# Kernel tuning notes

Measured on AMD Instinct MI355X. Metric: run time of the kernel, lower is better.

The kernel has to match this reference:

```python
import jax, jax.numpy as jnp
import numpy as np

N_SRC = 100000
N_DST = 20000
E = 640000
IN_FEATS = 256
NUM_HEADS = 4
OUT_FEATS = 32
NEG_SLOPE = 0.2


def setup_inputs() -> dict:
    key = jax.random.key(0)
    ks = jax.random.split(key, 8)
    x = jax.random.normal(ks[0], (N_SRC, IN_FEATS), dtype=jnp.float32)
    src_idx = jax.random.randint(ks[1], (E,), 0, N_SRC)
    dst_idx = jax.random.randint(ks[2], (E,), 0, N_DST)
    dst_to_src = jax.random.randint(ks[3], (N_DST,), 0, N_SRC)
    # parameters (xavier-ish scale)
    W = jax.random.normal(ks[4], (IN_FEATS, NUM_HEADS * OUT_FEATS), dtype=jnp.float32) * (1.0 / np.sqrt(IN_FEATS))
    attn_l = jax.random.normal(ks[5], (NUM_HEADS, OUT_FEATS), dtype=jnp.float32) * 0.1
    attn_r = jax.random.normal(ks[6], (NUM_HEADS, OUT_FEATS), dtype=jnp.float32) * 0.1
    return {"x": x, "W": W, "attn_l": attn_l, "attn_r": attn_r,
            "src_idx": src_idx, "dst_idx": dst_idx, "dst_to_src": dst_to_src}


def reference(x, W, attn_l, attn_r, src_idx, dst_idx, dst_to_src):
    # fc + reshape to heads: [N_src, H, D]
    h = (x @ W).reshape(N_SRC, NUM_HEADS, OUT_FEATS)
    # per-src-node left attention score: [N_src, H]
    el = jnp.einsum('nhd,hd->nh', h, attn_l)
    # self_gather: dst nodes are a subset of src nodes
    h_dst = h[dst_to_src]                       # [N_dst, H, D]
    er = jnp.einsum('nhd,hd->nh', h_dst, attn_r)  # [N_dst, H]
    # apply_edge + leaky_relu: per-edge scores [E, H]
    e = el[src_idx] + er[dst_idx]
    e = jnp.where(e >= 0, e, NEG_SLOPE * e)
    # NOTE: original code normalizes leaky_relu(e) directly (no exp)
    sum_e = jax.ops.segment_sum(e, dst_idx, num_segments=N_DST)  # [N_dst, H]
    attention = e / sum_e[dst_idx]              # [E, H]
    # attention_gather: weighted scatter-add of src features to dst
    msg = attention[:, :, None] * h[src_idx]    # [E, H, D]
    out = jax.ops.segment_sum(msg, dst_idx, num_segments=N_DST)  # [N_dst, H, D]
    return out
```

## Files before the change

### kernel.cpp

```cpp
#include <hip/hip_runtime.h>

#define N_SRC 100000
#define N_DST 20000
#define NE 640000
#define IN_F 256
#define NH 4
#define DF 32
#define NCOL 128

__global__ void k_prep(const float* __restrict__ W,
                       const float* __restrict__ attn_l,
                       const float* __restrict__ attn_r,
                       double* __restrict__ Wlr_t,
                       int* __restrict__ cnt) {
    int k = threadIdx.x;
    for (int j = 0; j < 8; ++j) {
        const float* attn = (j < 4) ? attn_l : attn_r;
        int hh = j & 3;
        double s = 0.0;
        for (int d = 0; d < DF; ++d)
            s += (double)W[k * NCOL + hh * DF + d] * (double)attn[hh * DF + d];
        Wlr_t[(size_t)j * IN_F + k] = s;
    }
    for (int i = k; i < N_DST; i += 256) cnt[i] = 0;
}

__global__ __launch_bounds__(512) void k_gemm(const float* __restrict__ x,
                                              const float* __restrict__ W,
                                              const double* __restrict__ Wlr_t,
                                              const int* __restrict__ dst_idx,
                                              float* __restrict__ h,
                                              double* __restrict__ el,
                                              int* __restrict__ cnt,
                                              int* __restrict__ rank) {
    __shared__ float xs[64][68];
    __shared__ double wlds[4][66];
    const int tid = threadIdx.x;
    const int row0 = blockIdx.x * 64;
    const int lane = tid & 63;
    const int cg = __builtin_amdgcn_readfirstlane(tid >> 6);
    const int c0 = cg * 16;
    const int srow = tid >> 3;
    const int shh = tid & 3;
    const int shalf = (tid >> 2) & 1;

    const int r_a = tid >> 4;
    const int r_b = 32 + (tid >> 4);
    const int q4 = (tid & 15) * 4;
    const int wj = tid >> 6, wk = tid & 63;

    float4 acc0 = make_float4(0.f, 0.f, 0.f, 0.f);
    float4 acc1 = make_float4(0.f, 0.f, 0.f, 0.f);
    float4 acc2 = make_float4(0.f, 0.f, 0.f, 0.f);
    float4 acc3 = make_float4(0.f, 0.f, 0.f, 0.f);
    double sacc = 0.0;

    float4 pf0 = make_float4(0.f, 0.f, 0.f, 0.f);
    float4 pf1 = make_float4(0.f, 0.f, 0.f, 0.f);
    double pfw = 0.0;
    if (row0 + r_a < N_SRC)
        pf0 = *((const float4*)(x + (size_t)(row0 + r_a) * IN_F + q4));
    if (row0 + r_b < N_SRC)
        pf1 = *((const float4*)(x + (size_t)(row0 + r_b) * IN_F + q4));
    if (tid < 256)
        pfw = Wlr_t[(size_t)wj * IN_F + wk];

    for (int chunk = 0; chunk < 4; ++chunk) {
        const int kbase = chunk * 64;
        if (chunk) __syncthreads();
        *((float4*)&xs[r_a][q4]) = pf0;
        *((float4*)&xs[r_b][q4]) = pf1;
        if (tid < 256) wlds[wj][wk] = pfw;
        __syncthreads();

        if (chunk < 3) {
            const int nk = kbase + 64;
            if (row0 + r_a < N_SRC)
                pf0 = *((const float4*)(x + (size_t)(row0 + r_a) * IN_F + nk + q4));
            if (row0 + r_b < N_SRC)
                pf1 = *((const float4*)(x + (size_t)(row0 + r_b) * IN_F + nk + q4));
            if (tid < 256)
                pfw = Wlr_t[(size_t)wj * IN_F + nk + wk];
        }

#pragma unroll 1
        for (int kq = 0; kq < 64; kq += 4) {
            const float* wp = W + (size_t)(kbase + kq) * NCOL + c0;
            float4 r0a = *((const float4*)(wp + 0));
            float4 r0b = *((const float4*)(wp + 4));
            float4 r0c = *((const float4*)(wp + 8));
            float4 r0d = *((const float4*)(wp + 12));
            float4 r1a = *((const float4*)(wp + NCOL + 0));
            float4 r1b = *((const float4*)(wp + NCOL + 4));
            float4 r1c = *((const float4*)(wp + NCOL + 8));
            float4 r1d = *((const float4*)(wp + NCOL + 12));
            float4 r2a = *((const float4*)(wp + 2 * NCOL + 0));
            float4 r2b = *((const float4*)(wp + 2 * NCOL + 4));
            float4 r2c = *((const float4*)(wp + 2 * NCOL + 8));
            float4 r2d = *((const float4*)(wp + 2 * NCOL + 12));
            float4 r3a = *((const float4*)(wp + 3 * NCOL + 0));
            float4 r3b = *((const float4*)(wp + 3 * NCOL + 4));
            float4 r3c = *((const float4*)(wp + 3 * NCOL + 8));
            float4 r3d = *((const float4*)(wp + 3 * NCOL + 12));
            float4 xv = *((const float4*)&xs[lane][kq]);
            acc0.x += xv.x * r0a.x + xv.y * r1a.x + xv.z * r2a.x + xv.w * r3a.x;
            acc0.y += xv.x * r0a.y + xv.y * r1a.y + xv.z * r2a.y + xv.w * r3a.y;
            acc0.z += xv.x * r0a.z + xv.y * r1a.z + xv.z * r2a.z + xv.w * r3a.z;
            acc0.w += xv.x * r0a.w + xv.y * r1a.w + xv.z * r2a.w + xv.w * r3a.w;
            acc1.x += xv.x * r0b.x + xv.y * r1b.x + xv.z * r2b.x + xv.w * r3b.x;
            acc1.y += xv.x * r0b.y + xv.y * r1b.y + xv.z * r2b.y + xv.w * r3b.y;
            acc1.z += xv.x * r0b.z + xv.y * r1b.z + xv.z * r2b.z + xv.w * r3b.z;
            acc1.w += xv.x * r0b.w + xv.y * r1b.w + xv.z * r2b.w + xv.w * r3b.w;
            acc2.x += xv.x * r0c.x + xv.y * r1c.x + xv.z * r2c.x + xv.w * r3c.x;
            acc2.y += xv.x * r0c.y + xv.y * r1c.y + xv.z * r2c.y + xv.w * r3c.y;
            acc2.z += xv.x * r0c.z + xv.y * r1c.z + xv.z * r2c.z + xv.w * r3c.z;
            acc2.w += xv.x * r0c.w + xv.y * r1c.w + xv.z * r2c.w + xv.w * r3c.w;
            acc3.x += xv.x * r0d.x + xv.y * r1d.x + xv.z * r2d.x + xv.w * r3d.x;
            acc3.y += xv.x * r0d.y + xv.y * r1d.y + xv.z * r2d.y + xv.w * r3d.y;
            acc3.z += xv.x * r0d.z + xv.y * r1d.z + xv.z * r2d.z + xv.w * r3d.z;
            acc3.w += xv.x * r0d.w + xv.y * r1d.w + xv.z * r2d.w + xv.w * r3d.w;
        }

        {
            const int kb = shalf * 32;
#pragma unroll 4
            for (int k = 0; k < 32; k += 4) {
                float4 xv = *((const float4*)&xs[srow][kb + k]);
                double2 wa = *((const double2*)&wlds[shh][kb + k]);
                double2 wb = *((const double2*)&wlds[shh][kb + k + 2]);
                sacc += (double)xv.x * wa.x + (double)xv.y * wa.y
                      + (double)xv.z * wb.x + (double)xv.w * wb.y;
            }
        }
    }

    {
        int row = row0 + lane;
        if (row < N_SRC) {
            float* hp = h + (size_t)row * NCOL + c0;
            *((float4*)(hp + 0)) = acc0;
            *((float4*)(hp + 4)) = acc1;
            *((float4*)(hp + 8)) = acc2;
            *((float4*)(hp + 12)) = acc3;
        }
    }

    sacc += __shfl_xor(sacc, 4);
    {
        int row = row0 + srow;
        if (shalf == 0 && row < N_SRC)
            el[(size_t)row * NH + shh] = sacc;
    }

    for (int e = blockIdx.x * 512 + tid; e < NE; e += gridDim.x * 512)
        rank[e] = atomicAdd(cnt + dst_idx[e], 1);
}

__global__ __launch_bounds__(1024) void k_scan(const int* __restrict__ cnt,
                                               int* __restrict__ offsets) {
    __shared__ int wsum[16];
    __shared__ int carry;
    int tid = threadIdx.x, lane = tid & 63, w = tid >> 6;
    if (tid == 0) carry = 0;
    __syncthreads();
    for (int base = 0; base < N_DST; base += 1024) {
        int i = base + tid;
        int v = (i < N_DST) ? cnt[i] : 0;
        int s = v;
#pragma unroll
        for (int off = 1; off < 64; off <<= 1) {
            int t = __shfl_up(s, off);
            if (lane >= off) s += t;
        }
        if (lane == 63) wsum[w] = s;
        __syncthreads();
        int wprefix = 0;
        for (int k = 0; k < w; ++k) wprefix += wsum[k];
        int incl = s + wprefix + carry;
        if (i < N_DST) offsets[i + 1] = incl;
        __syncthreads();
        if (tid == 1023) carry = incl;
        __syncthreads();
    }
    if (tid == 0) offsets[0] = 0;
}

__global__ __launch_bounds__(256) void k_fill(const int* __restrict__ src_idx,
                                              const int* __restrict__ dst_idx,
                                              const int* __restrict__ offsets,
                                              const int* __restrict__ rank,
                                              int* __restrict__ edge_src) {
    int gid = blockIdx.x * 256 + threadIdx.x;
    if (gid >= NE) return;
    int d = dst_idx[gid];
    edge_src[offsets[d] + rank[gid]] = src_idx[gid];
}

__global__ __launch_bounds__(256) void k_fused(const int* __restrict__ offsets,
                                               const int* __restrict__ edge_src,
                                               const double* __restrict__ el,
                                               const float* __restrict__ x,
                                               const double* __restrict__ Wlr_t,
                                               const int* __restrict__ dst_to_src,
                                               const float* __restrict__ h,
                                               float* __restrict__ out) {
    __shared__ double att_sh[4][4][68];
    __shared__ int    s_sh[4][64];

    const int w = threadIdx.x >> 6;
    const int lane = threadIdx.x & 63;
    const int d = blockIdx.x * 4 + w;
    if (d >= N_DST) return;
    const int beg = offsets[d];
    const int deg = offsets[d + 1] - beg;

    double er4[NH];
    {
        const int srcrow = dst_to_src[d];
        float4 xv = *((const float4*)(x + (size_t)srcrow * IN_F + lane * 4));
        const double xd[4] = {(double)xv.x, (double)xv.y, (double)xv.z, (double)xv.w};
#pragma unroll
        for (int hh = 0; hh < 4; ++hh) {
            const double* wp = Wlr_t + (size_t)(4 + hh) * IN_F + lane * 4;
            er4[hh] = xd[0] * wp[0] + xd[1] * wp[1] + xd[2] * wp[2] + xd[3] * wp[3];
        }
#pragma unroll
        for (int hh = 0; hh < 4; ++hh) {
#pragma unroll
            for (int m = 32; m >= 1; m >>= 1)
                er4[hh] += __shfl_xor(er4[hh], m);
        }
    }
    const double er0 = er4[0], er1 = er4[1], er2 = er4[2], er3 = er4[3];

    double sum0 = 0.0, sum1 = 0.0, sum2 = 0.0, sum3 = 0.0;
    double e0r = 0.0, e1r = 0.0, e2r = 0.0, e3r = 0.0;
    int s_first = 0;
    for (int j = lane; j < deg; j += 64) {
        int s = edge_src[beg + j];
        double2 ela = *((const double2*)(el + (size_t)s * NH));
        double2 elb = *((const double2*)(el + (size_t)s * NH + 2));
        double e0 = ela.x + er0; e0 = (e0 >= 0.0) ? e0 : 0.2 * e0;
        double e1 = ela.y + er1; e1 = (e1 >= 0.0) ? e1 : 0.2 * e1;
        double e2 = elb.x + er2; e2 = (e2 >= 0.0) ? e2 : 0.2 * e2;
        double e3 = elb.y + er3; e3 = (e3 >= 0.0) ? e3 : 0.2 * e3;
        sum0 += e0; sum1 += e1; sum2 += e2; sum3 += e3;
        if (j == lane) { s_first = s; e0r = e0; e1r = e1; e2r = e2; e3r = e3; }
    }
#pragma unroll
    for (int m = 32; m >= 1; m >>= 1) {
        sum0 += __shfl_xor(sum0, m);
        sum1 += __shfl_xor(sum1, m);
        sum2 += __shfl_xor(sum2, m);
        sum3 += __shfl_xor(sum3, m);
    }

    if (lane < deg) {
        s_sh[w][lane] = s_first;
        att_sh[w][0][lane] = e0r / sum0;
        att_sh[w][1][lane] = e1r / sum1;
        att_sh[w][2][lane] = e2r / sum2;
        att_sh[w][3][lane] = e3r / sum3;
    }

    const int js = lane >> 5;
    const int cq = lane & 31;
    const int hd = cq >> 3;
    const double Shd = (hd == 0) ? sum0 : (hd == 1) ? sum1 : (hd == 2) ? sum2 : sum3;
    const double erhd = (hd == 0) ? er0 : (hd == 1) ? er1 : (hd == 2) ? er2 : er3;

    double acc0 = 0.0, acc1 = 0.0, acc2 = 0.0, acc3 = 0.0;
    for (int j = js; j < deg; j += 2) {
        int s; double att;
        if (j < 64) {
            s = s_sh[w][j];
            att = att_sh[w][hd][j];
        } else {
            s = edge_src[beg + j];
            double e = el[(size_t)s * NH + hd] + erhd;
            e = (e >= 0.0) ? e : 0.2 * e;
            att = e / Shd;
        }
        float4 hv = *((const float4*)(h + (size_t)s * NCOL + cq * 4));
        acc0 += att * (double)hv.x;
        acc1 += att * (double)hv.y;
        acc2 += att * (double)hv.z;
        acc3 += att * (double)hv.w;
    }
    acc0 += __shfl_xor(acc0, 32);
    acc1 += __shfl_xor(acc1, 32);
    acc2 += __shfl_xor(acc2, 32);
    acc3 += __shfl_xor(acc3, 32);

    if (lane < 32) {
        *((float4*)(out + (size_t)d * NCOL + lane * 4)) =
            make_float4((float)acc0, (float)acc1, (float)acc2, (float)acc3);
    }
}

extern "C" void kernel_launch(void* const* d_in, const int* in_sizes, int n_in,
                              void* d_out, int out_size, void* d_ws, size_t ws_size,
                              hipStream_t stream) {
    const float* x      = (const float*)d_in[0];
    const float* W      = (const float*)d_in[1];
    const float* attn_l = (const float*)d_in[2];
    const float* attn_r = (const float*)d_in[3];
    const int* src_idx  = (const int*)d_in[4];
    const int* dst_idx  = (const int*)d_in[5];
    const int* dst_to_src = (const int*)d_in[6];
    float* out = (float*)d_out;

    char* p = (char*)d_ws;
    double* Wlr_t  = (double*)p;  p += (size_t)8 * IN_F * sizeof(double);
    double* el     = (double*)p;  p += (size_t)N_SRC * NH * sizeof(double);
    float*  h      = (float*)p;   p += (size_t)N_SRC * NCOL * sizeof(float);
    int*    cnt      = (int*)p;   p += (size_t)N_DST * sizeof(int);
    int*    offsets  = (int*)p;   p += (size_t)(N_DST + 1) * sizeof(int);
    int*    rank     = (int*)p;   p += (size_t)NE * sizeof(int);
    int*    edge_src = (int*)p;   p += (size_t)NE * sizeof(int);

    k_prep<<<1, 256, 0, stream>>>(W, attn_l, attn_r, Wlr_t, cnt);
    k_gemm<<<(N_SRC + 63) / 64, 512, 0, stream>>>(x, W, Wlr_t, dst_idx, h, el, cnt, rank);
    k_scan<<<1, 1024, 0, stream>>>(cnt, offsets);
    k_fill<<<(NE + 255) / 256, 256, 0, stream>>>(src_idx, dst_idx, offsets, rank, edge_src);
    k_fused<<<N_DST / 4, 256, 0, stream>>>(offsets, edge_src, el, x, Wlr_t, dst_to_src, h, out);
}
```

Measured before the change: 226.6 us.

## Stage W in LDS once per persistent block and loop over row tiles

The GEMM kernel now loads the full 256x128 weight matrix and the attention-projected weights into shared memory once per block, then runs a persistent grid of 256 blocks that loop over 64-row tiles. Before, every block streamed W from global memory (through the caches) inside its inner loop. The change is meant to cut repeated global and L2 traffic for W and the per-tile Wlr loads. In exchange it uses about 140KB of LDS per block, which allows only one block per CU, and it adds an extra barrier per chunk. With only 256 blocks, the edge-count atomic loop is also spread over fewer threads.

After: 289.3 us. 1.28x slower.

```diff
diff --git a/kernel.cpp b/kernel.cpp
--- a/kernel.cpp
+++ b/kernel.cpp
@@ -7,6 +7,7 @@
 #define NH 4
 #define DF 32
 #define NCOL 128
+#define NTILES ((N_SRC + 63) / 64)
 
 __global__ void k_prep(const float* __restrict__ W,
                        const float* __restrict__ attn_l,
@@ -33,10 +34,10 @@
                                               double* __restrict__ el,
                                               int* __restrict__ cnt,
                                               int* __restrict__ rank) {
+    __shared__ float wg[256][128];
     __shared__ float xs[64][68];
-    __shared__ double wlds[4][66];
+    __shared__ double wlds[4][258];
     const int tid = threadIdx.x;
-    const int row0 = blockIdx.x * 64;
     const int lane = tid & 63;
     const int cg = __builtin_amdgcn_readfirstlane(tid >> 6);
     const int c0 = cg * 16;
@@ -47,109 +48,117 @@
     const int r_a = tid >> 4;
     const int r_b = 32 + (tid >> 4);
     const int q4 = (tid & 15) * 4;
-    const int wj = tid >> 6, wk = tid & 63;
-
-    float4 acc0 = make_float4(0.f, 0.f, 0.f, 0.f);
-    float4 acc1 = make_float4(0.f, 0.f, 0.f, 0.f);
-    float4 acc2 = make_float4(0.f, 0.f, 0.f, 0.f);
-    float4 acc3 = make_float4(0.f, 0.f, 0.f, 0.f);
-    double sacc = 0.0;
-
-    float4 pf0 = make_float4(0.f, 0.f, 0.f, 0.f);
-    float4 pf1 = make_float4(0.f, 0.f, 0.f, 0.f);
-    double pfw = 0.0;
-    if (row0 + r_a < N_SRC)
-        pf0 = *((const float4*)(x + (size_t)(row0 + r_a) * IN_F + q4));
-    if (row0 + r_b < N_SRC)
-        pf1 = *((const float4*)(x + (size_t)(row0 + r_b) * IN_F + q4));
-    if (tid < 256)
-        pfw = Wlr_t[(size_t)wj * IN_F + wk];
-
-    for (int chunk = 0; chunk < 4; ++chunk) {
-        const int kbase = chunk * 64;
-        if (chunk) __syncthreads();
-        *((float4*)&xs[r_a][q4]) = pf0;
-        *((float4*)&xs[r_b][q4]) = pf1;
-        if (tid < 256) wlds[wj][wk] = pfw;
-        __syncthreads();
-
-        if (chunk < 3) {
-            const int nk = kbase + 64;
-            if (row0 + r_a < N_SRC)
-                pf0 = *((const float4*)(x + (size_t)(row0 + r_a) * IN_F + nk + q4));
-            if (row0 + r_b < N_SRC)
-                pf1 = *((const float4*)(x + (size_t)(row0 + r_b) * IN_F + nk + q4));
-            if (tid < 256)
-                pfw = Wlr_t[(size_t)wj * IN_F + nk + wk];
-        }
+
+    for (int i = tid; i < 256 * 32; i += 512) {
+        int kk = i >> 5, q = i & 31;
+        *((float4*)&wg[kk][q * 4]) = *((const float4*)(W + (size_t)kk * NCOL + q * 4));
+    }
+    for (int i = tid; i < 4 * IN_F; i += 512)
+        wlds[i >> 8][i & 255] = Wlr_t[(size_t)(i >> 8) * IN_F + (i & 255)];
+    __syncthreads();
+
+    for (int tile = blockIdx.x; tile < NTILES; tile += gridDim.x) {
+        const int row0 = tile * 64;
+
+        float4 acc0 = make_float4(0.f, 0.f, 0.f, 0.f);
+        float4 acc1 = make_float4(0.f, 0.f, 0.f, 0.f);
+        float4 acc2 = make_float4(0.f, 0.f, 0.f, 0.f);
+        float4 acc3 = make_float4(0.f, 0.f, 0.f, 0.f);
+        double sacc = 0.0;
+
+        float4 pf0 = make_float4(0.f, 0.f, 0.f, 0.f);
+        float4 pf1 = make_float4(0.f, 0.f, 0.f, 0.f);
+        if (row0 + r_a < N_SRC)
+            pf0 = *((const float4*)(x + (size_t)(row0 + r_a) * IN_F + q4));
+        if (row0 + r_b < N_SRC)
+            pf1 = *((const float4*)(x + (size_t)(row0 + r_b) * IN_F + q4));
+
+        for (int chunk = 0; chunk < 4; ++chunk) {
+            const int kbase = chunk * 64;
+            __syncthreads();
+            *((float4*)&xs[r_a][q4]) = pf0;
+            *((float4*)&xs[r_b][q4]) = pf1;
+            __syncthreads();
+
+            if (chunk < 3) {
+                const int nk = kbase + 64;
+                if (row0 + r_a < N_SRC)
+                    pf0 = *((const float4*)(x + (size_t)(row0 + r_a) * IN_F + nk + q4));
+                if (row0 + r_b < N_SRC)
+                    pf1 = *((const float4*)(x + (size_t)(row0 + r_b) * IN_F + nk + q4));
+            }
 
 #pragma unroll 1
-        for (int kq = 0; kq < 64; kq += 4) {
-            const float* wp = W + (size_t)(kbase + kq) * NCOL + c0;
-            float4 r0a = *((const float4*)(wp + 0));
-            float4 r0b = *((const float4*)(wp + 4));
-            float4 r0c = *((const float4*)(wp + 8));
-            float4 r0d = *((const float4*)(wp + 12));
-            float4 r1a = *((const float4*)(wp + NCOL + 0));
-            float4 r1b = *((const float4*)(wp + NCOL + 4));
-            float4 r1c = *((const float4*)(wp + NCOL + 8));
-            float4 r1d = *((const float4*)(wp + NCOL + 12));
-            float4 r2a = *((const float4*)(wp + 2 * NCOL + 0));
-            float4 r2b = *((const float4*)(wp + 2 * NCOL + 4));
-            float4 r2c = *((const float4*)(wp + 2 * NCOL + 8));
-            float4 r2d = *((const float4*)(wp + 2 * NCOL + 12));
-            float4 r3a = *((const float4*)(wp + 3 * NCOL + 0));
-            float4 r3b = *((const float4*)(wp + 3 * NCOL + 4));
-            float4 r3c = *((const float4*)(wp + 3 * NCOL + 8));
-            float4 r3d = *((const float4*)(wp + 3 * NCOL + 12));
-            float4 xv = *((const float4*)&xs[lane][kq]);
-            acc0.x += xv.x * r0a.x + xv.y * r1a.x + xv.z * r2a.x + xv.w * r3a.x;
-            acc0.y += xv.x * r0a.y + xv.y * r1a.y + xv.z * r2a.y + xv.w * r3a.y;
-            acc0.z += xv.x * r0a.z + xv.y * r1a.z + xv.z * r2a.z + xv.w * r3a.z;
-            acc0.w += xv.x * r0a.w + xv.y * r1a.w + xv.z * r2a.w + xv.w * r3a.w;
-            acc1.x += xv.x * r0b.x + xv.y * r1b.x + xv.z * r2b.x + xv.w * r3b.x;
-            acc1.y += xv.x * r0b.y + xv.y * r1b.y + xv.z * r2b.y + xv.w * r3b.y;
-            acc1.z += xv.x * r0b.z + xv.y * r1b.z + xv.z * r2b.z + xv.w * r3b.z;
-            acc1.w += xv.x * r0b.w + xv.y * r1b.w + xv.z * r2b.w + xv.w * r3b.w;
-            acc2.x += xv.x * r0c.x + xv.y * r1c.x + xv.z * r2c.x + xv.w * r3c.x;
-            acc2.y += xv.x * r0c.y + xv.y * r1c.y + xv.z * r2c.y + xv.w * r3c.y;
-            acc2.z += xv.x * r0c.z + xv.y * r1c.z + xv.z * r2c.z + xv.w * r3c.z;
-            acc2.w += xv.x * r0c.w + xv.y * r1c.w + xv.z * r2c.w + xv.w * r3c.w;
-            acc3.x += xv.x * r0d.x + xv.y * r1d.x + xv.z * r2d.x + xv.w * r3d.x;
-            acc3.y += xv.x * r0d.y + xv.y * r1d.y + xv.z * r2d.y + xv.w * r3d.y;
-            acc3.z += xv.x * r0d.z + xv.y * r1d.z + xv.z * r2d.z + xv.w * r3d.z;
-            acc3.w += xv.x * r0d.w + xv.y * r1d.w + xv.z * r2d.w + xv.w * r3d.w;
+            for (int kq = 0; kq < 64; kq += 4) {
+                const float* wp0 = &wg[kbase + kq + 0][c0];
+                const float* wp1 = &wg[kbase + kq + 1][c0];
+                const float* wp2 = &wg[kbase + kq + 2][c0];
+                const float* wp3 = &wg[kbase + kq + 3][c0];
+                float4 r0a = *((const float4*)(wp0 + 0));
+                float4 r0b = *((const float4*)(wp0 + 4));
+                float4 r0c = *((const float4*)(wp0 + 8));
+                float4 r0d = *((const float4*)(wp0 + 12));
+                float4 r1a = *((const float4*)(wp1 + 0));
+                float4 r1b = *((const float4*)(wp1 + 4));
+                float4 r1c = *((const float4*)(wp1 + 8));
+                float4 r1d = *((const float4*)(wp1 + 12));
+                float4 r2a = *((const float4*)(wp2 + 0));
+                float4 r2b = *((const float4*)(wp2 + 4));
+                float4 r2c = *((const float4*)(wp2 + 8));
+                float4 r2d = *((const float4*)(wp2 + 12));
+                float4 r3a = *((const float4*)(wp3 + 0));
+                float4 r3b = *((const float4*)(wp3 + 4));
+                float4 r3c = *((const float4*)(wp3 + 8));
+                float4 r3d = *((const float4*)(wp3 + 12));
+                float4 xv = *((const float4*)&xs[lane][kq]);
+                acc0.x += xv.x * r0a.x + xv.y * r1a.x + xv.z * r2a.x + xv.w * r3a.x;
+                acc0.y += xv.x * r0a.y + xv.y * r1a.y + xv.z * r2a.y + xv.w * r3a.y;
+                acc0.z += xv.x * r0a.z + xv.y * r1a.z + xv.z * r2a.z + xv.w * r3a.z;
+                acc0.w += xv.x * r0a.w + xv.y * r1a.w + xv.z * r2a.w + xv.w * r3a.w;
+                acc1.x += xv.x * r0b.x + xv.y * r1b.x + xv.z * r2b.x + xv.w * r3b.x;
+                acc1.y += xv.x * r0b.y + xv.y * r1b.y + xv.z * r2b.y + xv.w * r3b.y;
+                acc1.z += xv.x * r0b.z + xv.y * r1b.z + xv.z * r2b.z + xv.w * r3b.z;
+                acc1.w += xv.x * r0b.w + xv.y * r1b.w + xv.z * r2b.w + xv.w * r3b.w;
+                acc2.x += xv.x * r0c.x + xv.y * r1c.x + xv.z * r2c.x + xv.w * r3c.x;
+                acc2.y += xv.x * r0c.y + xv.y * r1c.y + xv.z * r2c.y + xv.w * r3c.y;
+                acc2.z += xv.x * r0c.z + xv.y * r1c.z + xv.z * r2c.z + xv.w * r3c.z;
+                acc2.w += xv.x * r0c.w + xv.y * r1c.w + xv.z * r2c.w + xv.w * r3c.w;
+                acc3.x += xv.x * r0d.x + xv.y * r1d.x + xv.z * r2d.x + xv.w * r3d.x;
+                acc3.y += xv.x * r0d.y + xv.y * r1d.y + xv.z * r2d.y + xv.w * r3d.y;
+                acc3.z += xv.x * r0d.z + xv.y * r1d.z + xv.z * r2d.z + xv.w * r3d.z;
+                acc3.w += xv.x * r0d.w + xv.y * r1d.w + xv.z * r2d.w + xv.w * r3d.w;
+            }
+
+            {
+                const int kb = shalf * 32;
+#pragma unroll 4
+                for (int k = 0; k < 32; k += 4) {
+                    float4 xv = *((const float4*)&xs[srow][kb + k]);
+                    double2 wa = *((const double2*)&wlds[shh][kbase + kb + k]);
+                    double2 wb = *((const double2*)&wlds[shh][kbase + kb + k + 2]);
+                    sacc += (double)xv.x * wa.x + (double)xv.y * wa.y
+                          + (double)xv.z * wb.x + (double)xv.w * wb.y;
+                }
+            }
         }
 
         {
-            const int kb = shalf * 32;
-#pragma unroll 4
-            for (int k = 0; k < 32; k += 4) {
-                float4 xv = *((const float4*)&xs[srow][kb + k]);
-                double2 wa = *((const double2*)&wlds[shh][kb + k]);
-                double2 wb = *((const double2*)&wlds[shh][kb + k + 2]);
-                sacc += (double)xv.x * wa.x + (double)xv.y * wa.y
-                      + (double)xv.z * wb.x + (double)xv.w * wb.y;
+            int row = row0 + lane;
+            if (row < N_SRC) {
+                float* hp = h + (size_t)row * NCOL + c0;
+                *((float4*)(hp + 0)) = acc0;
+                *((float4*)(hp + 4)) = acc1;
+                *((float4*)(hp + 8)) = acc2;
+                *((float4*)(hp + 12)) = acc3;
             }
         }
-    }
-
-    {
-        int row = row0 + lane;
-        if (row < N_SRC) {
-            float* hp = h + (size_t)row * NCOL + c0;
-            *((float4*)(hp + 0)) = acc0;
-            *((float4*)(hp + 4)) = acc1;
-            *((float4*)(hp + 8)) = acc2;
-            *((float4*)(hp + 12)) = acc3;
-        }
-    }
-
-    sacc += __shfl_xor(sacc, 4);
-    {
-        int row = row0 + srow;
-        if (shalf == 0 && row < N_SRC)
-            el[(size_t)row * NH + shh] = sacc;
+
+        sacc += __shfl_xor(sacc, 4);
+        {
+            int row = row0 + srow;
+            if (shalf == 0 && row < N_SRC)
+                el[(size_t)row * NH + shh] = sacc;
+        }
     }
 
     for (int e = blockIdx.x * 512 + tid; e < NE; e += gridDim.x * 512)
@@ -320,7 +329,7 @@
     int*    edge_src = (int*)p;   p += (size_t)NE * sizeof(int);
 
     k_prep<<<1, 256, 0, stream>>>(W, attn_l, attn_r, Wlr_t, cnt);
-    k_gemm<<<(N_SRC + 63) / 64, 512, 0, stream>>>(x, W, Wlr_t, dst_idx, h, el, cnt, rank);
+    k_gemm<<<256, 512, 0, stream>>>(x, W, Wlr_t, dst_idx, h, el, cnt, rank);
     k_scan<<<1, 1024, 0, stream>>>(cnt, offsets);
     k_fill<<<(NE + 255) / 256, 256, 0, stream>>>(src_idx, dst_idx, offsets, rank, edge_src);
     k_fused<<<N_DST / 4, 256, 0, stream>>>(offsets, edge_src, el, x, Wlr_t, dst_to_src, h, out);
```
